# Optimization experiments

Hardware: AMD Instinct MI355X
Metric: run time of the kernel (lower is better)

Reference implementation:

```python
import jax, jax.numpy as jnp
import numpy as np

NUM_USER, NUM_ITEM, NUM_TIME = 200000, 100000, 5000
P, Q, R = 32, 32, 32
N = 131072


def _xavier(key, shape):
    fan_in, fan_out = shape[0], int(np.prod(shape[1:]))
    limit = float(np.sqrt(6.0 / (fan_in + fan_out)))
    return jax.random.uniform(key, shape, dtype=jnp.float32, minval=-limit, maxval=limit)


def setup_inputs() -> dict:
    key = jax.random.key(0)
    k1, k2, k3, k4, k5, k6, k7 = jax.random.split(key, 7)
    return {
        "i_input": jax.random.randint(k1, (N,), 0, NUM_USER),
        "j_input": jax.random.randint(k2, (N,), 0, NUM_ITEM),
        "k_input": jax.random.randint(k3, (N,), 0, NUM_TIME),
        "user_embeddings": _xavier(k4, (NUM_USER, P)),
        "item_embeddings": _xavier(k5, (NUM_ITEM, Q)),
        "time_embeddings": _xavier(k6, (NUM_TIME, R)),
        "core_tensor": _xavier(k7, (P, Q, R)),
    }


def reference(i_input, j_input, k_input, user_embeddings, item_embeddings,
              time_embeddings, core_tensor):
    # Gather per-sample embeddings: [n,p], [n,q], [n,r]
    i_embeds = user_embeddings[i_input]
    j_embeds = item_embeddings[j_input]
    k_embeds = time_embeddings[k_input]
    # Fused Tucker contraction: never materialize the (n,p,q,r) outer product.
    # Mathematically identical to einsum('np,nq,nr,pqr->n', ...).
    t = jnp.einsum('np,pqr->nqr', i_embeds, core_tensor)  # [n,q,r]
    t = jnp.einsum('nqr,nq->nr', t, j_embeds)             # [n,r]
    return jnp.einsum('nr,nr->n', t, k_embeds)            # [n]
```

## Files before the change

### kernel.cpp

```cpp
#include <hip/hip_runtime.h>


#define BIN_CAP 128

__device__ __forceinline__ void build_H_body(const float* __restrict__ G,
                                             const float* __restrict__ W,
                                             float* __restrict__ H,
                                             int num_time, int bblk) {
    const int pq4 = threadIdx.x;
    const int kbase = bblk * 8;

    float acc[8][4];
#pragma unroll
    for (int kk = 0; kk < 8; ++kk)
#pragma unroll
        for (int i = 0; i < 4; ++i) acc[kk][i] = 0.f;

#pragma unroll
    for (int r4 = 0; r4 < 8; ++r4) {
        float4 g[4];
#pragma unroll
        for (int i = 0; i < 4; ++i)
            g[i] = *(const float4*)(G + (size_t)(pq4 * 4 + i) * 32 + r4 * 4);
#pragma unroll
        for (int kk = 0; kk < 8; ++kk) {
            int k = kbase + kk;
            int kc = (k < num_time) ? k : (num_time - 1);
            float4 w = *(const float4*)(W + (size_t)kc * 32 + r4 * 4);
#pragma unroll
            for (int i = 0; i < 4; ++i)
                acc[kk][i] += g[i].x * w.x + g[i].y * w.y + g[i].z * w.z + g[i].w * w.w;
        }
    }

#pragma unroll
    for (int kk = 0; kk < 8; ++kk) {
        int k = kbase + kk;
        if (k < num_time) {
            float4 o = make_float4(acc[kk][0], acc[kk][1], acc[kk][2], acc[kk][3]);
            *(float4*)(H + (size_t)k * 1024 + pq4 * 4) = o;
        }
    }
}

__device__ __forceinline__ void scatter_body(const int* __restrict__ K,
                                             const int* __restrict__ I,
                                             const int* __restrict__ J,
                                             int* __restrict__ counts,
                                             int4* __restrict__ bins,
                                             int* __restrict__ ovf_cnt,
                                             int4* __restrict__ ovf,
                                             int n, int sblk, int nsblk) {
    for (int idx = sblk * 256 + (int)threadIdx.x; idx < n; idx += nsblk * 256) {
        int k = K[idx];
        int4 rec = make_int4(idx, I[idx], J[idx], k);
        int pos = atomicAdd(&counts[k], 1);
        if (pos < BIN_CAP) {
            bins[(size_t)k * BIN_CAP + pos] = rec;
        } else {
            int o = atomicAdd(ovf_cnt, 1);
            ovf[o] = rec;
        }
    }
}

__global__ __launch_bounds__(256) void fused_prepare(
        const float* __restrict__ G, const float* __restrict__ W,
        float* __restrict__ H,
        const int* __restrict__ K, const int* __restrict__ I,
        const int* __restrict__ J, int* __restrict__ counts,
        int4* __restrict__ bins, int* __restrict__ ovf_cnt,
        int4* __restrict__ ovf, int n, int num_time,
        int nbuild, int nscatter) {
    const int b = blockIdx.x;
    if (b < nbuild) {
        build_H_body(G, W, H, num_time, b);
    } else {
        scatter_body(K, I, J, counts, bins, ovf_cnt, ovf, n, b - nbuild, nscatter);
    }
}

__global__ __launch_bounds__(256) void build_H(const float* __restrict__ G,
                                               const float* __restrict__ W,
                                               float* __restrict__ H,
                                               int num_time) {
    build_H_body(G, W, H, num_time, blockIdx.x);
}

__global__ __launch_bounds__(256) void tucker_eval_grouped(
        const float* __restrict__ U, const float* __restrict__ V,
        const float* __restrict__ H, const int* __restrict__ counts,
        const int4* __restrict__ bins, float* __restrict__ out,
        int num_time, const int* __restrict__ ovf_cnt,
        const int4* __restrict__ ovf) {
    __shared__ float4 Hs4[4][256];
    const int wave = threadIdx.x >> 6;
    const int lane = threadIdx.x & 63;
    const int k = blockIdx.x * 4 + wave;
    const int qq = lane & 7;
    const int s8 = lane >> 3;

    int m = 0;
    if (k < num_time) {
        const float4* __restrict__ Hrow4 = (const float4*)(H + (size_t)k * 1024);
#pragma unroll
        for (int c = 0; c < 4; ++c)
            Hs4[wave][lane + 64 * c] = Hrow4[lane + 64 * c];
        m = counts[k];
        m = (m < BIN_CAP) ? m : BIN_CAP;
    }
    __syncthreads();

    if (k < num_time && m > 0) {
        const int iters = (m + 7) >> 3;
        const float4* __restrict__ Hw = Hs4[wave];
        const int4* __restrict__ bbase = bins + (size_t)k * BIN_CAP;

        int4 myrec = bbase[(lane < m) ? lane : (m - 1)];

        int src0 = s8;
        if (src0 >= m) src0 = m - 1;
        int rn = __shfl(myrec.x, src0, 64);
        int ri = __shfl(myrec.y, src0, 64);
        int rj = __shfl(myrec.z, src0, 64);
        float4 u0[8];
        {
            const float4* __restrict__ Ur = (const float4*)(U + (size_t)ri * 32);
#pragma unroll
            for (int p4 = 0; p4 < 8; ++p4) u0[p4] = Ur[p4];
        }
        float4 v0 = ((const float4*)(V + (size_t)rj * 32))[qq];
        int outn = rn;

        for (int t = 0; t < iters; ++t) {
            float4 u1[8];
            float4 v1;
            int outn_n = 0;
            const int tn = t + 1;
            if (tn < iters) {
                int sn = tn * 8 + s8;
                if (sn >= m) sn = m - 1;
                int ni, nj;
                if (sn < 64) {
                    outn_n = __shfl(myrec.x, sn, 64);
                    ni = __shfl(myrec.y, sn, 64);
                    nj = __shfl(myrec.z, sn, 64);
                } else {
                    int4 r = bbase[sn];
                    outn_n = r.x; ni = r.y; nj = r.z;
                }
                const float4* __restrict__ Urn = (const float4*)(U + (size_t)ni * 32);
#pragma unroll
                for (int p4 = 0; p4 < 8; ++p4) u1[p4] = Urn[p4];
                v1 = ((const float4*)(V + (size_t)nj * 32))[qq];
            }

            float4 acc = make_float4(0.f, 0.f, 0.f, 0.f);
#pragma unroll
            for (int p4 = 0; p4 < 8; ++p4) {
                float4 h;
                h = Hw[(p4 * 4 + 0) * 8 + qq];
                acc.x += u0[p4].x * h.x; acc.y += u0[p4].x * h.y;
                acc.z += u0[p4].x * h.z; acc.w += u0[p4].x * h.w;
                h = Hw[(p4 * 4 + 1) * 8 + qq];
                acc.x += u0[p4].y * h.x; acc.y += u0[p4].y * h.y;
                acc.z += u0[p4].y * h.z; acc.w += u0[p4].y * h.w;
                h = Hw[(p4 * 4 + 2) * 8 + qq];
                acc.x += u0[p4].z * h.x; acc.y += u0[p4].z * h.y;
                acc.z += u0[p4].z * h.z; acc.w += u0[p4].z * h.w;
                h = Hw[(p4 * 4 + 3) * 8 + qq];
                acc.x += u0[p4].w * h.x; acc.y += u0[p4].w * h.y;
                acc.z += u0[p4].w * h.z; acc.w += u0[p4].w * h.w;
            }
            float sd = acc.x * v0.x + acc.y * v0.y + acc.z * v0.z + acc.w * v0.w;
            sd += __shfl_xor(sd, 1, 64);
            sd += __shfl_xor(sd, 2, 64);
            sd += __shfl_xor(sd, 4, 64);
            const int s = t * 8 + s8;
            if (s < m && qq == 0) out[outn] = sd;

            if (tn < iters) {
#pragma unroll
                for (int p4 = 0; p4 < 8; ++p4) u0[p4] = u1[p4];
                v0 = v1;
                outn = outn_n;
            }
        }
    }

    const int cnt = *ovf_cnt;
    if (cnt > 0) {
        const int gwave = (int)blockIdx.x * 4 + wave;
        const int nw = (int)gridDim.x * 4;
        const int pg = lane >> 3;
        for (int s = gwave; s < cnt; s += nw) {
            int4 rec = ovf[s];
            const float4* __restrict__ Hrow = (const float4*)(H + (size_t)rec.w * 1024);
            const float* __restrict__ Ur = U + (size_t)rec.y * 32;

            float4 acc = make_float4(0.f, 0.f, 0.f, 0.f);
#pragma unroll
            for (int it = 0; it < 4; ++it) {
                float4 h = Hrow[lane + it * 64];
                float up = Ur[pg + it * 8];
                acc.x += up * h.x; acc.y += up * h.y;
                acc.z += up * h.z; acc.w += up * h.w;
            }
#pragma unroll
            for (int off = 8; off < 64; off <<= 1) {
                acc.x += __shfl_xor(acc.x, off, 64);
                acc.y += __shfl_xor(acc.y, off, 64);
                acc.z += __shfl_xor(acc.z, off, 64);
                acc.w += __shfl_xor(acc.w, off, 64);
            }
            float4 v4 = ((const float4*)(V + (size_t)rec.z * 32))[qq];
            float sd = acc.x * v4.x + acc.y * v4.y + acc.z * v4.z + acc.w * v4.w;
            sd += __shfl_xor(sd, 1, 64);
            sd += __shfl_xor(sd, 2, 64);
            sd += __shfl_xor(sd, 4, 64);
            if (lane == 0) out[rec.x] = sd;
        }
    }
}

__global__ __launch_bounds__(256) void tucker_eval(const int* __restrict__ I,
                                                   const int* __restrict__ J,
                                                   const int* __restrict__ K,
                                                   const float* __restrict__ U,
                                                   const float* __restrict__ V,
                                                   const float* __restrict__ H,
                                                   float* __restrict__ out,
                                                   int n_samples) {
    const int wave = (int)((blockIdx.x * (unsigned)blockDim.x + threadIdx.x) >> 6);
    const int lane = threadIdx.x & 63;
    if (wave >= n_samples) return;
    const int i = I[wave];
    const int j = J[wave];
    const int k = K[wave];
    const int qq = lane & 7;
    const int pg = lane >> 3;
    const float4* __restrict__ Hrow = (const float4*)(H + (size_t)k * 1024);
    const float* __restrict__ Urow = U + (size_t)i * 32;
    float4 acc = make_float4(0.f, 0.f, 0.f, 0.f);
#pragma unroll
    for (int it = 0; it < 4; ++it) {
        float4 h = Hrow[lane + it * 64];
        float up = Urow[pg + it * 8];
        acc.x += up * h.x; acc.y += up * h.y;
        acc.z += up * h.z; acc.w += up * h.w;
    }
#pragma unroll
    for (int off = 8; off < 64; off <<= 1) {
        acc.x += __shfl_xor(acc.x, off, 64);
        acc.y += __shfl_xor(acc.y, off, 64);
        acc.z += __shfl_xor(acc.z, off, 64);
        acc.w += __shfl_xor(acc.w, off, 64);
    }
    float4 v4 = ((const float4*)(V + (size_t)j * 32))[qq];
    float s = acc.x * v4.x + acc.y * v4.y + acc.z * v4.z + acc.w * v4.w;
    s += __shfl_xor(s, 1, 64);
    s += __shfl_xor(s, 2, 64);
    s += __shfl_xor(s, 4, 64);
    if (lane == 0) out[wave] = s;
}

__global__ __launch_bounds__(256) void tucker_direct(const int* __restrict__ I,
                                                     const int* __restrict__ J,
                                                     const int* __restrict__ K,
                                                     const float* __restrict__ U,
                                                     const float* __restrict__ V,
                                                     const float* __restrict__ W,
                                                     const float* __restrict__ G,
                                                     float* __restrict__ out,
                                                     int n_samples) {
    __shared__ float Gc[4 * 32 * 32];
    const int n = blockIdx.x * blockDim.x + threadIdx.x;
    const bool active = (n < n_samples);
    int i = 0, j = 0, k = 0;
    if (active) { i = I[n]; j = J[n]; k = K[n]; }
    float4 w4[8];
#pragma unroll
    for (int r4 = 0; r4 < 8; ++r4)
        w4[r4] = ((const float4*)(W + (size_t)k * 32))[r4];
    float v[32];
#pragma unroll
    for (int q4 = 0; q4 < 8; ++q4) {
        float4 t = ((const float4*)(V + (size_t)j * 32))[q4];
        v[q4 * 4 + 0] = t.x; v[q4 * 4 + 1] = t.y;
        v[q4 * 4 + 2] = t.z; v[q4 * 4 + 3] = t.w;
    }
    const float* __restrict__ Urow = U + (size_t)i * 32;
    float acc = 0.f;
    for (int c = 0; c < 8; ++c) {
        __syncthreads();
#pragma unroll
        for (int t = 0; t < 4; ++t) {
            int idx = threadIdx.x + t * 256;
            ((float4*)Gc)[idx] = ((const float4*)(G + (size_t)c * 4096))[idx];
        }
        __syncthreads();
        for (int pp = 0; pp < 4; ++pp) {
            float up = Urow[c * 4 + pp];
#pragma unroll
            for (int q = 0; q < 32; ++q) {
                float t0 = 0.f;
#pragma unroll
                for (int r4 = 0; r4 < 8; ++r4) {
                    float4 g = ((const float4*)Gc)[pp * 256 + q * 8 + r4];
                    t0 += g.x * w4[r4].x + g.y * w4[r4].y + g.z * w4[r4].z + g.w * w4[r4].w;
                }
                acc += up * v[q] * t0;
            }
        }
    }
    if (active) out[n] = acc;
}

extern "C" void kernel_launch(void* const* d_in, const int* in_sizes, int n_in,
                              void* d_out, int out_size, void* d_ws, size_t ws_size,
                              hipStream_t stream) {
    const int*   I = (const int*)d_in[0];
    const int*   J = (const int*)d_in[1];
    const int*   K = (const int*)d_in[2];
    const float* U = (const float*)d_in[3];
    const float* V = (const float*)d_in[4];
    const float* W = (const float*)d_in[5];
    const float* G = (const float*)d_in[6];
    float* out = (float*)d_out;

    const int n_samples = in_sizes[0];
    const int num_time = in_sizes[5] / 32;

    const size_t h_bytes = (size_t)num_time * 1024 * sizeof(float);
    const size_t z_bytes = (size_t)(num_time + 1) * sizeof(int);
    const size_t z_pad = (z_bytes + 15) & ~(size_t)15;
    const size_t bins_bytes = (size_t)num_time * BIN_CAP * sizeof(int4);
    const size_t ovf_bytes = (size_t)n_samples * sizeof(int4);
    const size_t need_full = h_bytes + z_pad + bins_bytes + ovf_bytes;

    if (ws_size >= need_full) {
        float* H       = (float*)d_ws;
        int*   counts  = (int*)((char*)d_ws + h_bytes);
        int*   ovf_cnt = counts + num_time;
        int4*  bins    = (int4*)((char*)d_ws + h_bytes + z_pad);
        int4*  ovf     = (int4*)((char*)d_ws + h_bytes + z_pad + bins_bytes);

        const int nbuild = (num_time + 7) / 8;
        const int nscatter = 512;

        hipMemsetAsync(counts, 0, z_bytes, stream);
        fused_prepare<<<nbuild + nscatter, 256, 0, stream>>>(
            G, W, H, K, I, J, counts, bins, ovf_cnt, ovf,
            n_samples, num_time, nbuild, nscatter);
        tucker_eval_grouped<<<(num_time + 3) / 4, 256, 0, stream>>>(
            U, V, H, counts, bins, out, num_time, ovf_cnt, ovf);
    } else if (ws_size >= h_bytes) {
        float* H = (float*)d_ws;
        build_H<<<(num_time + 7) / 8, 256, 0, stream>>>(G, W, H, num_time);
        const long long total_threads = (long long)n_samples * 64;
        tucker_eval<<<(int)((total_threads + 255) / 256), 256, 0, stream>>>(
            I, J, K, U, V, H, out, n_samples);
    } else {
        tucker_direct<<<(n_samples + 255) / 256, 256, 0, stream>>>(
            I, J, K, U, V, W, G, out, n_samples);
    }
}
```

Measured before the change: 132.1 us.

## Fuse H construction into eval kernel, computing H rows directly into shared memory

Removes the global H buffer (5000x1024 floats) by computing each block's four H rows from the core tensor and time embeddings directly into LDS inside the eval kernel. The scatter becomes its own kernel. This avoids writing and re-reading roughly 20 MB of H through global memory, and the bin-record and U/V loads are issued before the barrier so they overlap with the H compute. Overflow samples are now handled per wave by scanning the whole overflow list and keeping only those matching its time index. That scan is cheap when the list is empty but serializes badly if bins overflow.

Measured after the change: 138.0 us. 4.4% more time.

```diff
diff --git a/kernel.cpp b/kernel.cpp
--- a/kernel.cpp
+++ b/kernel.cpp
@@ -3,55 +3,16 @@
 
 #define BIN_CAP 128
 
-__device__ __forceinline__ void build_H_body(const float* __restrict__ G,
-                                             const float* __restrict__ W,
-                                             float* __restrict__ H,
-                                             int num_time, int bblk) {
-    const int pq4 = threadIdx.x;
-    const int kbase = bblk * 8;
-
-    float acc[8][4];
-#pragma unroll
-    for (int kk = 0; kk < 8; ++kk)
-#pragma unroll
-        for (int i = 0; i < 4; ++i) acc[kk][i] = 0.f;
-
-#pragma unroll
-    for (int r4 = 0; r4 < 8; ++r4) {
-        float4 g[4];
-#pragma unroll
-        for (int i = 0; i < 4; ++i)
-            g[i] = *(const float4*)(G + (size_t)(pq4 * 4 + i) * 32 + r4 * 4);
-#pragma unroll
-        for (int kk = 0; kk < 8; ++kk) {
-            int k = kbase + kk;
-            int kc = (k < num_time) ? k : (num_time - 1);
-            float4 w = *(const float4*)(W + (size_t)kc * 32 + r4 * 4);
-#pragma unroll
-            for (int i = 0; i < 4; ++i)
-                acc[kk][i] += g[i].x * w.x + g[i].y * w.y + g[i].z * w.z + g[i].w * w.w;
-        }
-    }
-
-#pragma unroll
-    for (int kk = 0; kk < 8; ++kk) {
-        int k = kbase + kk;
-        if (k < num_time) {
-            float4 o = make_float4(acc[kk][0], acc[kk][1], acc[kk][2], acc[kk][3]);
-            *(float4*)(H + (size_t)k * 1024 + pq4 * 4) = o;
-        }
-    }
-}
-
-__device__ __forceinline__ void scatter_body(const int* __restrict__ K,
-                                             const int* __restrict__ I,
-                                             const int* __restrict__ J,
-                                             int* __restrict__ counts,
-                                             int4* __restrict__ bins,
-                                             int* __restrict__ ovf_cnt,
-                                             int4* __restrict__ ovf,
-                                             int n, int sblk, int nsblk) {
-    for (int idx = sblk * 256 + (int)threadIdx.x; idx < n; idx += nsblk * 256) {
+__global__ __launch_bounds__(256) void scatter_k(const int* __restrict__ K,
+                                                 const int* __restrict__ I,
+                                                 const int* __restrict__ J,
+                                                 int* __restrict__ counts,
+                                                 int4* __restrict__ bins,
+                                                 int* __restrict__ ovf_cnt,
+                                                 int4* __restrict__ ovf,
+                                                 int n) {
+    for (int idx = blockIdx.x * blockDim.x + threadIdx.x; idx < n;
+         idx += gridDim.x * blockDim.x) {
         int k = K[idx];
         int4 rec = make_int4(idx, I[idx], J[idx], k);
         int pos = atomicAdd(&counts[k], 1);
@@ -64,73 +25,81 @@
     }
 }
 
-__global__ __launch_bounds__(256) void fused_prepare(
-        const float* __restrict__ G, const float* __restrict__ W,
-        float* __restrict__ H,
-        const int* __restrict__ K, const int* __restrict__ I,
-        const int* __restrict__ J, int* __restrict__ counts,
-        int4* __restrict__ bins, int* __restrict__ ovf_cnt,
-        int4* __restrict__ ovf, int n, int num_time,
-        int nbuild, int nscatter) {
-    const int b = blockIdx.x;
-    if (b < nbuild) {
-        build_H_body(G, W, H, num_time, b);
-    } else {
-        scatter_body(K, I, J, counts, bins, ovf_cnt, ovf, n, b - nbuild, nscatter);
-    }
-}
-
-__global__ __launch_bounds__(256) void build_H(const float* __restrict__ G,
-                                               const float* __restrict__ W,
-                                               float* __restrict__ H,
-                                               int num_time) {
-    build_H_body(G, W, H, num_time, blockIdx.x);
-}
-
-__global__ __launch_bounds__(256) void tucker_eval_grouped(
+__global__ __launch_bounds__(256) void tucker_eval_fused(
         const float* __restrict__ U, const float* __restrict__ V,
-        const float* __restrict__ H, const int* __restrict__ counts,
-        const int4* __restrict__ bins, float* __restrict__ out,
-        int num_time, const int* __restrict__ ovf_cnt,
-        const int4* __restrict__ ovf) {
+        const float* __restrict__ W, const float* __restrict__ G,
+        const int* __restrict__ counts, const int4* __restrict__ bins,
+        float* __restrict__ out, int num_time,
+        const int* __restrict__ ovf_cnt, const int4* __restrict__ ovf) {
     __shared__ float4 Hs4[4][256];
-    const int wave = threadIdx.x >> 6;
-    const int lane = threadIdx.x & 63;
-    const int k = blockIdx.x * 4 + wave;
+    const int tid = threadIdx.x;
+    const int wave = tid >> 6;
+    const int lane = tid & 63;
+    const int kb = (int)blockIdx.x * 4;
+    const int k = kb + wave;
     const int qq = lane & 7;
     const int s8 = lane >> 3;
 
     int m = 0;
     if (k < num_time) {
-        const float4* __restrict__ Hrow4 = (const float4*)(H + (size_t)k * 1024);
-#pragma unroll
-        for (int c = 0; c < 4; ++c)
-            Hs4[wave][lane + 64 * c] = Hrow4[lane + 64 * c];
         m = counts[k];
         m = (m < BIN_CAP) ? m : BIN_CAP;
     }
-    __syncthreads();
-
-    if (k < num_time && m > 0) {
-        const int iters = (m + 7) >> 3;
-        const float4* __restrict__ Hw = Hs4[wave];
-        const int4* __restrict__ bbase = bins + (size_t)k * BIN_CAP;
-
-        int4 myrec = bbase[(lane < m) ? lane : (m - 1)];
-
-        int src0 = s8;
-        if (src0 >= m) src0 = m - 1;
-        int rn = __shfl(myrec.x, src0, 64);
+    const int kc_bins = (k < num_time) ? k : (num_time - 1);
+    const int4* __restrict__ bbase = bins + (size_t)kc_bins * BIN_CAP;
+    int4 myrec = bbase[lane];
+
+    {
+        float acc[4][4];
+#pragma unroll
+        for (int kk = 0; kk < 4; ++kk)
+#pragma unroll
+            for (int i = 0; i < 4; ++i) acc[kk][i] = 0.f;
+
+        const float4* __restrict__ G4 = (const float4*)G;
+#pragma unroll
+        for (int r4 = 0; r4 < 8; ++r4) {
+            float4 g[4];
+#pragma unroll
+            for (int i = 0; i < 4; ++i)
+                g[i] = G4[(size_t)(4 * tid + i) * 8 + r4];
+#pragma unroll
+            for (int kk = 0; kk < 4; ++kk) {
+                int kc = kb + kk;
+                kc = (kc < num_time) ? kc : (num_time - 1);
+                float4 w = ((const float4*)(W + (size_t)kc * 32))[r4];
+#pragma unroll
+                for (int i = 0; i < 4; ++i)
+                    acc[kk][i] += g[i].x * w.x + g[i].y * w.y +
+                                  g[i].z * w.z + g[i].w * w.w;
+            }
+        }
+#pragma unroll
+        for (int kk = 0; kk < 4; ++kk)
+            Hs4[kk][tid] = make_float4(acc[kk][0], acc[kk][1],
+                                       acc[kk][2], acc[kk][3]);
+    }
+
+    float4 u0[8];
+    float4 v0 = make_float4(0.f, 0.f, 0.f, 0.f);
+    int outn = 0;
+    const bool active = (k < num_time) && (m > 0);
+    if (active) {
+        int src0 = (s8 < m) ? s8 : (m - 1);
+        outn   = __shfl(myrec.x, src0, 64);
         int ri = __shfl(myrec.y, src0, 64);
         int rj = __shfl(myrec.z, src0, 64);
-        float4 u0[8];
-        {
-            const float4* __restrict__ Ur = (const float4*)(U + (size_t)ri * 32);
-#pragma unroll
-            for (int p4 = 0; p4 < 8; ++p4) u0[p4] = Ur[p4];
-        }
-        float4 v0 = ((const float4*)(V + (size_t)rj * 32))[qq];
-        int outn = rn;
+        const float4* __restrict__ Ur = (const float4*)(U + (size_t)ri * 32);
+#pragma unroll
+        for (int p4 = 0; p4 < 8; ++p4) u0[p4] = Ur[p4];
+        v0 = ((const float4*)(V + (size_t)rj * 32))[qq];
+    }
+
+    __syncthreads();
+
+    const float4* __restrict__ Hw = Hs4[wave];
+    if (active) {
+        const int iters = (m + 7) >> 3;
 
         for (int t = 0; t < iters; ++t) {
             float4 u1[8];
@@ -188,37 +157,77 @@
         }
     }
 
-    const int cnt = *ovf_cnt;
-    if (cnt > 0) {
-        const int gwave = (int)blockIdx.x * 4 + wave;
-        const int nw = (int)gridDim.x * 4;
-        const int pg = lane >> 3;
-        for (int s = gwave; s < cnt; s += nw) {
-            int4 rec = ovf[s];
-            const float4* __restrict__ Hrow = (const float4*)(H + (size_t)rec.w * 1024);
-            const float* __restrict__ Ur = U + (size_t)rec.y * 32;
-
-            float4 acc = make_float4(0.f, 0.f, 0.f, 0.f);
-#pragma unroll
-            for (int it = 0; it < 4; ++it) {
-                float4 h = Hrow[lane + it * 64];
-                float up = Ur[pg + it * 8];
-                acc.x += up * h.x; acc.y += up * h.y;
-                acc.z += up * h.z; acc.w += up * h.w;
-            }
-#pragma unroll
-            for (int off = 8; off < 64; off <<= 1) {
-                acc.x += __shfl_xor(acc.x, off, 64);
-                acc.y += __shfl_xor(acc.y, off, 64);
-                acc.z += __shfl_xor(acc.z, off, 64);
-                acc.w += __shfl_xor(acc.w, off, 64);
-            }
-            float4 v4 = ((const float4*)(V + (size_t)rec.z * 32))[qq];
-            float sd = acc.x * v4.x + acc.y * v4.y + acc.z * v4.z + acc.w * v4.w;
-            sd += __shfl_xor(sd, 1, 64);
-            sd += __shfl_xor(sd, 2, 64);
-            sd += __shfl_xor(sd, 4, 64);
-            if (lane == 0) out[rec.x] = sd;
+    if (k < num_time) {
+        const int cnt = *ovf_cnt;
+        if (cnt > 0) {
+            const int pg = lane >> 3;
+            for (int s = 0; s < cnt; ++s) {
+                int4 rec = ovf[s];
+                if (rec.w != k) continue;
+                const float* __restrict__ Ur2 = U + (size_t)rec.y * 32;
+                float4 acc = make_float4(0.f, 0.f, 0.f, 0.f);
+#pragma unroll
+                for (int it = 0; it < 4; ++it) {
+                    float4 h = Hw[lane + it * 64];
+                    float up = Ur2[pg + it * 8];
+                    acc.x += up * h.x; acc.y += up * h.y;
+                    acc.z += up * h.z; acc.w += up * h.w;
+                }
+#pragma unroll
+                for (int off = 8; off < 64; off <<= 1) {
+                    acc.x += __shfl_xor(acc.x, off, 64);
+                    acc.y += __shfl_xor(acc.y, off, 64);
+                    acc.z += __shfl_xor(acc.z, off, 64);
+                    acc.w += __shfl_xor(acc.w, off, 64);
+                }
+                float4 v4 = ((const float4*)(V + (size_t)rec.z * 32))[qq];
+                float sd = acc.x * v4.x + acc.y * v4.y +
+                           acc.z * v4.z + acc.w * v4.w;
+                sd += __shfl_xor(sd, 1, 64);
+                sd += __shfl_xor(sd, 2, 64);
+                sd += __shfl_xor(sd, 4, 64);
+                if (lane == 0) out[rec.x] = sd;
+            }
+        }
+    }
+}
+
+__global__ __launch_bounds__(256) void build_H(const float* __restrict__ G,
+                                               const float* __restrict__ W,
+                                               float* __restrict__ H,
+                                               int num_time) {
+    const int pq4 = threadIdx.x;
+    const int kbase = blockIdx.x * 8;
+
+    float acc[8][4];
+#pragma unroll
+    for (int kk = 0; kk < 8; ++kk)
+#pragma unroll
+        for (int i = 0; i < 4; ++i) acc[kk][i] = 0.f;
+
+#pragma unroll
+    for (int r4 = 0; r4 < 8; ++r4) {
+        float4 g[4];
+#pragma unroll
+        for (int i = 0; i < 4; ++i)
+            g[i] = *(const float4*)(G + (size_t)(pq4 * 4 + i) * 32 + r4 * 4);
+#pragma unroll
+        for (int kk = 0; kk < 8; ++kk) {
+            int k = kbase + kk;
+            int kc = (k < num_time) ? k : (num_time - 1);
+            float4 w = *(const float4*)(W + (size_t)kc * 32 + r4 * 4);
+#pragma unroll
+            for (int i = 0; i < 4; ++i)
+                acc[kk][i] += g[i].x * w.x + g[i].y * w.y + g[i].z * w.z + g[i].w * w.w;
+        }
+    }
+
+#pragma unroll
+    for (int kk = 0; kk < 8; ++kk) {
+        int k = kbase + kk;
+        if (k < num_time) {
+            float4 o = make_float4(acc[kk][0], acc[kk][1], acc[kk][2], acc[kk][3]);
+            *(float4*)(H + (size_t)k * 1024 + pq4 * 4) = o;
         }
     }
 }
@@ -339,21 +348,16 @@
     const size_t need_full = h_bytes + z_pad + bins_bytes + ovf_bytes;
 
     if (ws_size >= need_full) {
-        float* H       = (float*)d_ws;
         int*   counts  = (int*)((char*)d_ws + h_bytes);
         int*   ovf_cnt = counts + num_time;
         int4*  bins    = (int4*)((char*)d_ws + h_bytes + z_pad);
         int4*  ovf     = (int4*)((char*)d_ws + h_bytes + z_pad + bins_bytes);
 
-        const int nbuild = (num_time + 7) / 8;
-        const int nscatter = 512;
-
         hipMemsetAsync(counts, 0, z_bytes, stream);
-        fused_prepare<<<nbuild + nscatter, 256, 0, stream>>>(
-            G, W, H, K, I, J, counts, bins, ovf_cnt, ovf,
-            n_samples, num_time, nbuild, nscatter);
-        tucker_eval_grouped<<<(num_time + 3) / 4, 256, 0, stream>>>(
-            U, V, H, counts, bins, out, num_time, ovf_cnt, ovf);
+        scatter_k<<<512, 256, 0, stream>>>(K, I, J, counts, bins, ovf_cnt, ovf,
+                                           n_samples);
+        tucker_eval_fused<<<(num_time + 3) / 4, 256, 0, stream>>>(
+            U, V, W, G, counts, bins, out, num_time, ovf_cnt, ovf);
     } else if (ws_size >= h_bytes) {
         float* H = (float*)d_ws;
         build_H<<<(num_time + 7) / 8, 256, 0, stream>>>(G, W, H, num_time);
```
